# Kernel tuning notes

Measured on AMD Instinct MI355X. Metric: run time of the kernel, lower is better.

## Reference

```python
import jax, jax.numpy as jnp
import numpy as np

BUCKET_SIZE = 64
N_HASHES = 8
TOKEN_SELF_ATTN_VALUE = -50000.0


def setup_inputs() -> dict:
    key = jax.random.key(0)
    k1, k2, k3, k4 = jax.random.split(key, 4)
    b, t, h, e = 2, 4096, 8, 64
    n_buckets = t // BUCKET_SIZE  # 64
    return {
        "qk": jax.random.normal(k1, (b, t, h, e), dtype=jnp.float32),
        "k": jax.random.normal(k2, (b, t, h, e), dtype=jnp.float32),
        "v": jax.random.normal(k3, (b, t, h, e), dtype=jnp.float32),
        # shared rotations: (dim, n_hashes, n_buckets // 2)
        "rotations": jax.random.normal(k4, (e, N_HASHES, n_buckets // 2), dtype=jnp.float32),
    }


def _look_one_back(x):
    # cat([x[:, -1:], x[:, :-1]], 1) == roll by 1 along chunk axis
    return jnp.concatenate([x, jnp.roll(x, 1, axis=1)], axis=2)


def reference(qk, k, v, rotations):
    b, t, h, e = qk.shape
    # 'b t h e -> (b h) t e'
    qk_m = qk.transpose(0, 2, 1, 3).reshape(b * h, t, e)
    v_m = v.transpose(0, 2, 1, 3).reshape(b * h, t, v.shape[-1])
    B, seqlen, dim = qk_m.shape
    dv = v_m.shape[-1]
    n_buckets = seqlen // BUCKET_SIZE

    # --- LSH hashing ---
    rot = jnp.einsum('btf,fhi->bhti', qk_m, rotations)  # (B, n_hashes, T, nb/2)
    rot = jnp.concatenate([rot, -rot], axis=-1)
    buckets = jnp.argmax(rot, axis=-1)                  # (B, n_hashes, T)
    offsets = (jnp.arange(N_HASHES) * n_buckets)[None, :, None]
    buckets = (buckets + offsets).reshape(B, -1)        # (B, n_hashes*T)

    # --- sort by bucket (keys are unique, so order is deterministic) ---
    ticker = jnp.arange(N_HASHES * seqlen)[None, :]
    buckets_and_t = seqlen * buckets + (ticker % seqlen)
    sticker = jnp.argsort(buckets_and_t, axis=-1)
    undo_sort = jnp.argsort(sticker, axis=-1)
    st = sticker % seqlen

    sqk = jnp.take_along_axis(qk_m, st[:, :, None], axis=1)
    sv = jnp.take_along_axis(v_m, st[:, :, None], axis=1)

    chunk = N_HASHES * n_buckets
    bq_t = st.reshape(B, chunk, -1)                     # (B, C, bs)
    bq = sqk.reshape(B, chunk, -1, dim)                 # (B, C, bs, e)
    bv = sv.reshape(B, chunk, -1, dv)

    # normalized keys (F.normalize with eps=1e-12)
    norm = jnp.maximum(jnp.linalg.norm(bq, axis=-1, keepdims=True), 1e-12)
    bk = bq / norm

    bk = _look_one_back(bk)
    bv2 = _look_one_back(bv)
    bkv_t = _look_one_back(bq_t)

    dots = jnp.einsum('bcie,bcje->bcij', bq, bk)        # (B, C, bs, 2*bs)
    self_mask = bq_t[:, :, :, None] == bkv_t[:, :, None, :]
    dots = jnp.where(self_mask, TOKEN_SELF_ATTN_VALUE, dots)

    lse = jax.nn.logsumexp(dots, axis=-1, keepdims=True)
    p = jnp.exp(dots - lse)
    bo = jnp.einsum('bcij,bcjd->bcid', p, bv2)

    so = bo.reshape(B, -1, dv)
    slogits = lse.reshape(B, -1)
    o = jnp.take_along_axis(so, undo_sort[:, :, None], axis=1)
    logits = jnp.take_along_axis(slogits, undo_sort, axis=1)

    o = o.reshape(B, N_HASHES, seqlen, dv)
    logits = logits.reshape(B, N_HASHES, seqlen, 1)

    # combine across hash rounds by softmax over round logsumexps
    probs = jnp.exp(logits - jax.nn.logsumexp(logits, axis=1, keepdims=True))
    out = jnp.sum(o * probs, axis=1)                    # (b*h, T, dv)
    return out
```

## Files before the change

### kernel.cpp

```cpp
#include <hip/hip_runtime.h>
#include <stdint.h>

#define BHN 16
#define TLEN 4096
#define EDIM 64
#define NHASH 8
#define NBUCK 64
#define GBUCK 512
#define NCHUNK 512
#define NITEMS 32768

#define WS_BUCKETS 0u
#define WS_SORTED  557056u
#define WS_LSE     2654208u
#define WS_O       4751360u
#define WS_QK16    71860224u
#define WS_V16     80248832u
#define WS_NQ      88637440u
#define WS_RTH     114065408u
#define WS_RTM     114098176u
#define WS_RTL     114130944u

typedef __attribute__((ext_vector_type(4))) float f32x4;
typedef __attribute__((ext_vector_type(8))) _Float16 f16x8;
typedef __attribute__((ext_vector_type(4))) _Float16 f16x4;
typedef __attribute__((ext_vector_type(4))) unsigned u32x4;

#define LOG2E 1.44269504088896f
#define LN2   0.69314718055995f
#define S11   4.8828125e-4f
#define S22   2.384185791015625e-7f

static __device__ __forceinline__ void split3(float x, _Float16& h0, _Float16& m0, _Float16& l0) {
  h0 = (_Float16)x;
  float r1 = x - (float)h0;
  m0 = (_Float16)(r1 * 2048.0f);
  float r2 = r1 - (float)m0 * (1.0f / 2048.0f);
  l0 = (_Float16)(r2 * 4194304.0f);
}

__global__ __launch_bounds__(128) void k_prep(const float* __restrict__ qk,
                                              const float* __restrict__ vin,
                                              const float* __restrict__ rot,
                                              _Float16* __restrict__ qk16n,
                                              _Float16* __restrict__ v16,
                                              float* __restrict__ nq,
                                              _Float16* __restrict__ rth,
                                              _Float16* __restrict__ rtm,
                                              _Float16* __restrict__ rtl) {
  int blk = blockIdx.x;
  int tid = threadIdx.x;

  if (blk == 8192) {
#pragma unroll
    for (int rep = 0; rep < 2; ++rep) {
      int n = tid + rep * 128;
      for (int f = 0; f < 64; ++f) {
        float x = rot[f * 256 + n];
        _Float16 h0, m0, l0;
        split3(x, h0, m0, l0);
        rth[n * 64 + f] = h0;
        rtm[n * 64 + f] = m0;
        rtl[n * 64 + f] = l0;
      }
    }
    return;
  }

  int b = blk >> 12, t = blk & 4095;
  int h = tid >> 4, e4 = tid & 15;

  size_t in_base = ((size_t)((b * 4096 + t) * 8 + h)) * 64 + e4 * 4;
  float4 qv = *(const float4*)(qk + in_base);
  float ss = qv.x * qv.x + qv.y * qv.y + qv.z * qv.z + qv.w * qv.w;
  ss += __shfl_xor(ss, 1);
  ss += __shfl_xor(ss, 2);
  ss += __shfl_xor(ss, 4);
  ss += __shfl_xor(ss, 8);
  float nrm = fmaxf(sqrtf(ss), 1e-12f);
  float inv = 1.f / nrm;

  size_t out_base = ((size_t)((b * 8 + h) * 4096 + t)) * 64 + e4 * 4;
  f16x4 qh;
  qh[0] = (_Float16)(qv.x * inv); qh[1] = (_Float16)(qv.y * inv);
  qh[2] = (_Float16)(qv.z * inv); qh[3] = (_Float16)(qv.w * inv);
  *(f16x4*)(qk16n + out_base) = qh;
  if (e4 == 0) nq[(size_t)(b * 8 + h) * 4096 + t] = nrm * LOG2E;

  float4 vv = *(const float4*)(vin + in_base);
  f16x4 vh;
  vh[0] = (_Float16)vv.x; vh[1] = (_Float16)vv.y;
  vh[2] = (_Float16)vv.z; vh[3] = (_Float16)vv.w;
  *(f16x4*)(v16 + out_base) = vh;
}

__global__ __launch_bounds__(256) void k_hash2(const float* __restrict__ qk,
                                               const _Float16* __restrict__ rth,
                                               const _Float16* __restrict__ rtm,
                                               const _Float16* __restrict__ rtl,
                                               uint8_t* __restrict__ buckets) {
  __shared__ __attribute__((aligned(16))) _Float16 ah[64 * 64];
  __shared__ __attribute__((aligned(16))) _Float16 am[64 * 64];
  __shared__ __attribute__((aligned(16))) _Float16 al[64 * 64];

  int tid = threadIdx.x;
  int bh = blockIdx.x >> 6;
  int tt = blockIdx.x & 63;
  int b = bh >> 3, head = bh & 7;

  {
    int r = tid & 63, fq = tid >> 6;
    const float4* src = (const float4*)(qk +
        ((size_t)((b * 4096 + tt * 64 + r) * 8 + head)) * 64 + fq * 16);
    float x[16];
#pragma unroll
    for (int i = 0; i < 4; ++i) {
      float4 v = src[i];
      x[4 * i + 0] = v.x; x[4 * i + 1] = v.y;
      x[4 * i + 2] = v.z; x[4 * i + 3] = v.w;
    }
    int s0 = fq * 2, rx = r & 7;
#pragma unroll
    for (int g8 = 0; g8 < 2; ++g8) {
      f16x8 hv, mv, lv;
#pragma unroll
      for (int e = 0; e < 8; ++e) {
        _Float16 h0, m0, l0;
        split3(x[g8 * 8 + e], h0, m0, l0);
        hv[e] = h0; mv[e] = m0; lv[e] = l0;
      }
      int off = r * 64 + (((s0 + g8) ^ rx) << 3);
      *(f16x8*)&ah[off] = hv;
      *(f16x8*)&am[off] = mv;
      *(f16x8*)&al[off] = lv;
    }
  }
  __syncthreads();

  int w = tid >> 6, l = tid & 63;
  int col = l & 15, kg = l >> 4;

  float bv[4][4];
  int   bi[4][4];

#pragma unroll
  for (int nt = 0; nt < 4; ++nt) {
    int nrow = w * 64 + nt * 16 + col;
    const _Float16* bh_p = rth + nrow * 64 + kg * 8;
    const _Float16* bm_p = rtm + nrow * 64 + kg * 8;
    const _Float16* bl_p = rtl + nrow * 64 + kg * 8;
    f16x8 Bh0 = *(const f16x8*)(bh_p),      Bh1 = *(const f16x8*)(bh_p + 32);
    f16x8 Bm0 = *(const f16x8*)(bm_p),      Bm1 = *(const f16x8*)(bm_p + 32);
    f16x8 Bl0 = *(const f16x8*)(bl_p),      Bl1 = *(const f16x8*)(bl_p + 32);

    f32x4 C0[4], C1[4], C2[4];
#pragma unroll
    for (int mt = 0; mt < 4; ++mt) {
      C0[mt] = (f32x4){0.f, 0.f, 0.f, 0.f};
      C1[mt] = (f32x4){0.f, 0.f, 0.f, 0.f};
      C2[mt] = (f32x4){0.f, 0.f, 0.f, 0.f};
    }

    __builtin_amdgcn_s_setprio(1);
#pragma unroll
    for (int mt = 0; mt < 4; ++mt) {
      int ar = mt * 16 + col, arx = ar & 7;
#pragma unroll
      for (int kh = 0; kh < 2; ++kh) {
        int slot = kh * 4 + kg;
        f16x8 Ah = *(f16x8*)&ah[ar * 64 + ((slot ^ arx) << 3)];
        f16x8 Am = *(f16x8*)&am[ar * 64 + ((slot ^ arx) << 3)];
        f16x8 Al = *(f16x8*)&al[ar * 64 + ((slot ^ arx) << 3)];
        f16x8 Bh = kh ? Bh1 : Bh0;
        f16x8 Bm = kh ? Bm1 : Bm0;
        f16x8 Bl = kh ? Bl1 : Bl0;
        C2[mt] = __builtin_amdgcn_mfma_f32_16x16x32_f16(Ah, Bl, C2[mt], 0, 0, 0);
        C2[mt] = __builtin_amdgcn_mfma_f32_16x16x32_f16(Al, Bh, C2[mt], 0, 0, 0);
        C2[mt] = __builtin_amdgcn_mfma_f32_16x16x32_f16(Am, Bm, C2[mt], 0, 0, 0);
        C1[mt] = __builtin_amdgcn_mfma_f32_16x16x32_f16(Ah, Bm, C1[mt], 0, 0, 0);
        C1[mt] = __builtin_amdgcn_mfma_f32_16x16x32_f16(Am, Bh, C1[mt], 0, 0, 0);
        C0[mt] = __builtin_amdgcn_mfma_f32_16x16x32_f16(Ah, Bh, C0[mt], 0, 0, 0);
      }
    }
    __builtin_amdgcn_s_setprio(0);

    int ib = (nt & 1) * 16 + col;
#pragma unroll
    for (int mt = 0; mt < 4; ++mt) {
#pragma unroll
      for (int r = 0; r < 4; ++r) {
        float V = C0[mt][r] + C1[mt][r] * S11 + C2[mt][r] * S22;
        float av = fabsf(V);
        int fi = (V >= 0.f) ? ib : ib + 32;
        if ((nt & 1) == 0) {
          bv[mt][r] = av; bi[mt][r] = fi;
        } else {
          if (av > bv[mt][r] || (av == bv[mt][r] && fi < bi[mt][r])) {
            bv[mt][r] = av; bi[mt][r] = fi;
          }
        }
      }
    }

    if (nt & 1) {
      int h = w * 2 + (nt >> 1);
#pragma unroll
      for (int mt = 0; mt < 4; ++mt) {
#pragma unroll
        for (int r = 0; r < 4; ++r) {
          float v = bv[mt][r]; int i_ = bi[mt][r];
#pragma unroll
          for (int d = 1; d < 16; d <<= 1) {
            float ov = __shfl_xor(v, d);
            int   oi = __shfl_xor(i_, d);
            if (ov > v || (ov == v && oi < i_)) { v = ov; i_ = oi; }
          }
          if (col == 0) {
            int t = tt * 64 + mt * 16 + kg * 4 + r;
            buckets[(bh * 8 + h) * 4096 + t] = (uint8_t)i_;
          }
        }
      }
    }
  }
}

__global__ __launch_bounds__(64) void k_sort(const uint8_t* __restrict__ buckets,
                                             int* __restrict__ sorted) {
  __shared__ uint8_t bkt[4096];
  __shared__ uint8_t lrk[4096];
  __shared__ int hist[64 * 65];
  __shared__ int sbase[64];
  int tid = threadIdx.x;
  int bh = blockIdx.x >> 3, h = blockIdx.x & 7;

  const int* src = (const int*)(buckets + (size_t)(bh * 8 + h) * 4096);
  for (int k = tid; k < 1024; k += 64) ((int*)bkt)[k] = src[k];
  for (int k = tid; k < 64 * 65; k += 64) hist[k] = 0;
  __syncthreads();

  {
    int c = tid;
    for (int k = 0; k < 64; ++k) {
      int t = c * 64 + k;
      int bin = bkt[t];
      int r = hist[c * 65 + bin];
      hist[c * 65 + bin] = r + 1;
      lrk[t] = (uint8_t)r;
    }
  }
  __syncthreads();

  int run = 0;
  {
    int bb = tid;
    for (int c2 = 0; c2 < 64; ++c2) {
      int val = hist[c2 * 65 + bb];
      hist[c2 * 65 + bb] = run;
      run += val;
    }
  }
  {
    int ex = run;
#pragma unroll
    for (int d = 1; d < 64; d <<= 1) {
      int o = __shfl_up(ex, d);
      if (tid >= d) ex += o;
    }
    ex -= run;
    sbase[tid] = h * 4096 + ex;
  }
  __syncthreads();

  {
    int c = tid;
    int* dst = sorted + (size_t)bh * 32768;
    for (int k = 0; k < 64; ++k) {
      int t = c * 64 + k;
      int bin = bkt[t];
      int pos = sbase[bin] + hist[c * 65 + bin] + (int)lrk[t];
      dst[pos] = h * 4096 + t;
    }
  }
}

__global__ __launch_bounds__(256, 4) void k_attn(const _Float16* __restrict__ qk16n,
                                                 const _Float16* __restrict__ v16,
                                                 const float* __restrict__ nq,
                                                 const int* __restrict__ sorted,
                                                 _Float16* __restrict__ o_buf,
                                                 float* __restrict__ lse_buf) {
  __shared__ __attribute__((aligned(16))) _Float16 kf[128 * 64];
  __shared__ __attribute__((aligned(16))) _Float16 vt[64 * 128];
  __shared__ __attribute__((aligned(16))) float pinv_s[64];
  __shared__ __attribute__((aligned(16))) int tv[128];
  __shared__ __attribute__((aligned(16))) int items[64];

  int tid = threadIdx.x;
  int bh = blockIdx.x & 15;
  int c  = blockIdx.x >> 4;

  if (tid < 128) {
    int r = tid;
    int pos = (r < 64) ? (c * 64 + r) : (((c + 511) & 511) * 64 + (r - 64));
    int item = sorted[(size_t)bh * 32768 + pos];
    tv[r] = item & 4095;
    if (r < 64) items[r] = item;
  }
  __syncthreads();

  int w = tid >> 6;
  int l = tid & 63;
  int col = l & 15;
  int kg = l >> 4;
  int rq = w * 16 + col;
  int rqx7 = rq & 7, rqx15 = rq & 15;
  int tq = tv[rq];
  float nqv = nq[(size_t)bh * 4096 + tq];

  {
    int r = tid >> 1, half = tid & 1;
    int t = tv[r];
    const f16x8* src = (const f16x8*)(qk16n + ((size_t)(bh * 4096 + t)) * 64 + half * 32);
    f16x8 d0 = src[0], d1 = src[1], d2 = src[2], d3 = src[3];
    int rx = r & 7, s0 = half * 4;
    *(f16x8*)&kf[r * 64 + (((s0 + 0) ^ rx) << 3)] = d0;
    *(f16x8*)&kf[r * 64 + (((s0 + 1) ^ rx) << 3)] = d1;
    *(f16x8*)&kf[r * 64 + (((s0 + 2) ^ rx) << 3)] = d2;
    *(f16x8*)&kf[r * 64 + (((s0 + 3) ^ rx) << 3)] = d3;
  }

  {
    int jp = tid & 63, db = tid >> 6, f0 = db * 16;
    int t0 = tv[2 * jp], t1 = tv[2 * jp + 1];
    const u32x4* s0p = (const u32x4*)(v16 + ((size_t)(bh * 4096 + t0)) * 64 + f0);
    const u32x4* s1p = (const u32x4*)(v16 + ((size_t)(bh * 4096 + t1)) * 64 + f0);
    u32x4 lo0 = s0p[0], hi0 = s0p[1];
    u32x4 lo1 = s1p[0], hi1 = s1p[1];
    int jbase = ((jp >> 2));
    int joff = (jp & 3) << 1;
#pragma unroll
    for (int i = 0; i < 16; ++i) {
      int d = f0 + i;
      unsigned a = (i < 8) ? lo0[(i >> 1) & 3] : hi0[(i >> 1) & 3];
      unsigned bsrc = (i < 8) ? lo1[(i >> 1) & 3] : hi1[(i >> 1) & 3];
      unsigned sel = (i & 1) ? 0x07060302u : 0x05040100u;
      unsigned pack = __builtin_amdgcn_perm(bsrc, a, sel);
      *(unsigned*)&vt[d * 128 + ((jbase ^ (d & 15)) << 3) + joff] = pack;
    }
  }
  __syncthreads();

  f16x8 qf[2];
#pragma unroll
  for (int ks = 0; ks < 2; ++ks)
    qf[ks] = *(f16x8*)&kf[rq * 64 + (((ks * 4 + kg) ^ rqx7) << 3)];

  f32x4 S[8];
#pragma unroll
  for (int mt = 0; mt < 8; ++mt) S[mt] = (f32x4){0.f, 0.f, 0.f, 0.f};

  __builtin_amdgcn_s_setprio(1);
#pragma unroll
  for (int mt = 0; mt < 8; ++mt) {
    int rj = mt * 16 + col;
    int rjx = rj & 7;
#pragma unroll
    for (int ks = 0; ks < 2; ++ks) {
      f16x8 a = *(f16x8*)&kf[rj * 64 + (((ks * 4 + kg) ^ rjx) << 3)];
      S[mt] = __builtin_amdgcn_mfma_f32_16x16x32_f16(a, qf[ks], S[mt], 0, 0, 0);
    }
  }
  __builtin_amdgcn_s_setprio(0);

  float vals[32];
  float mx = -1e30f;
#pragma unroll
  for (int mt = 0; mt < 8; ++mt) {
    int j0 = mt * 16 + kg * 4;
    int4 tk4 = *(int4*)&tv[j0];
    int tki[4] = {tk4.x, tk4.y, tk4.z, tk4.w};
#pragma unroll
    for (int r = 0; r < 4; ++r) {
      float d = S[mt][r] * nqv;
      if (tki[r] == tq) d = -50000.0f * LOG2E;
      vals[mt * 4 + r] = d;
      mx = fmaxf(mx, d);
    }
  }
  mx = fmaxf(mx, __shfl_xor(mx, 16));
  mx = fmaxf(mx, __shfl_xor(mx, 32));
  float ssum = 0.f;
#pragma unroll
  for (int i = 0; i < 32; ++i) {
    float e = __builtin_amdgcn_exp2f(vals[i] - mx);
    vals[i] = e;
    ssum += e;
  }
  ssum += __shfl_xor(ssum, 16);
  ssum += __shfl_xor(ssum, 32);
  if (kg == 0) {
    int item = items[rq];
    lse_buf[((size_t)bh * 4096 + (item & 4095)) * 8 + (item >> 12)] =
        (mx + __builtin_amdgcn_logf(ssum)) * LN2;
    pinv_s[rq] = 1.f / ssum;
  }

  __syncthreads();

  _Float16* Pb = kf;
#pragma unroll
  for (int mt = 0; mt < 8; ++mt) {
    int j0 = mt * 16 + kg * 4;
    int slot = j0 >> 3;
    int off = rq * 128 + ((slot ^ rqx15) << 3) + ((kg & 1) << 2);
    f16x4 pk;
#pragma unroll
    for (int r = 0; r < 4; ++r) pk[r] = (_Float16)vals[mt * 4 + r];
    *(f16x4*)&Pb[off] = pk;
  }
  asm volatile("s_waitcnt lgkmcnt(0)" ::: "memory");

  f32x4 O[4];
#pragma unroll
  for (int nt = 0; nt < 4; ++nt) O[nt] = (f32x4){0.f, 0.f, 0.f, 0.f};
  __builtin_amdgcn_s_setprio(1);
#pragma unroll
  for (int ks = 0; ks < 4; ++ks) {
    int slot = (ks << 2) + kg;
    f16x8 pa = *(f16x8*)&Pb[rq * 128 + ((slot ^ rqx15) << 3)];
#pragma unroll
    for (int nt = 0; nt < 4; ++nt) {
      int dD = nt * 16 + col;
      f16x8 vb = *(f16x8*)&vt[dD * 128 + ((slot ^ (dD & 15)) << 3)];
      O[nt] = __builtin_amdgcn_mfma_f32_16x16x32_f16(pa, vb, O[nt], 0, 0, 0);
    }
  }
  __builtin_amdgcn_s_setprio(0);

  {
    int i0 = w * 16 + kg * 4;
    int4 it4 = *(int4*)&items[i0];
    float4 pv4 = *(float4*)&pinv_s[i0];
    int iti[4] = {it4.x, it4.y, it4.z, it4.w};
    float pvi[4] = {pv4.x, pv4.y, pv4.z, pv4.w};
#pragma unroll
    for (int r = 0; r < 4; ++r) {
      int item = iti[r];
      _Float16* orow = o_buf +
          (((size_t)bh * 4096 + (item & 4095)) * 8 + (item >> 12)) * 64;
#pragma unroll
      for (int nt = 0; nt < 4; ++nt) orow[nt * 16 + col] = (_Float16)(O[nt][r] * pvi[r]);
    }
  }
}

__global__ __launch_bounds__(256) void k_combine(const _Float16* __restrict__ o_buf,
                                                 const float* __restrict__ lse_buf,
                                                 float* __restrict__ out) {
  int gid = blockIdx.x * 256 + threadIdx.x;
  int d4 = gid & 15;
  int t  = (gid >> 4) & 4095;
  int bh = gid >> 16;

  const float* lrow = lse_buf + ((size_t)bh * 4096 + t) * 8;
  float lx[8];
#pragma unroll
  for (int h = 0; h < 8; ++h) lx[h] = lrow[h];
  float m = lx[0];
#pragma unroll
  for (int h = 1; h < 8; ++h) m = fmaxf(m, lx[h]);
  float wv[8]; float s = 0.f;
#pragma unroll
  for (int h = 0; h < 8; ++h) { wv[h] = __expf(lx[h] - m); s += wv[h]; }
  float inv = 1.f / s;

  const _Float16* obase = o_buf + ((size_t)bh * 4096 + t) * 8 * 64 + d4 * 4;
  float ax = 0.f, ay = 0.f, az = 0.f, aw = 0.f;
#pragma unroll
  for (int h = 0; h < 8; ++h) {
    f16x4 ov = *(const f16x4*)(obase + h * 64);
    ax = fmaf(wv[h], (float)ov[0], ax);
    ay = fmaf(wv[h], (float)ov[1], ay);
    az = fmaf(wv[h], (float)ov[2], az);
    aw = fmaf(wv[h], (float)ov[3], aw);
  }
  *(float4*)(out + ((size_t)(bh * 4096 + t)) * 64 + d4 * 4) =
      make_float4(ax * inv, ay * inv, az * inv, aw * inv);
}

extern "C" void kernel_launch(void* const* d_in, const int* in_sizes, int n_in,
                              void* d_out, int out_size, void* d_ws, size_t ws_size,
                              hipStream_t stream) {
  const float* qk  = (const float*)d_in[0];
  const float* vin = (const float*)d_in[2];
  const float* rot = (const float*)d_in[3];

  uint8_t* ws = (uint8_t*)d_ws;
  uint8_t*  buckets = ws + WS_BUCKETS;
  int*      sorted  = (int*)(ws + WS_SORTED);
  float*    lse_buf = (float*)(ws + WS_LSE);
  _Float16* o_buf   = (_Float16*)(ws + WS_O);
  _Float16* qk16n   = (_Float16*)(ws + WS_QK16);
  _Float16* v16     = (_Float16*)(ws + WS_V16);
  float*    nqbuf   = (float*)(ws + WS_NQ);
  _Float16* rth     = (_Float16*)(ws + WS_RTH);
  _Float16* rtm     = (_Float16*)(ws + WS_RTM);
  _Float16* rtl     = (_Float16*)(ws + WS_RTL);
  float*    out     = (float*)d_out;

  k_prep<<<8193, 128, 0, stream>>>(qk, vin, rot, qk16n, v16, nqbuf, rth, rtm, rtl);
  k_hash2<<<BHN * 64, 256, 0, stream>>>(qk, rth, rtm, rtl, buckets);
  k_sort<<<BHN * NHASH, 64, 0, stream>>>(buckets, sorted);
  k_attn<<<BHN * NCHUNK, 256, 0, stream>>>(qk16n, v16, nqbuf, sorted, o_buf, lse_buf);
  k_combine<<<4096, 256, 0, stream>>>(o_buf, lse_buf, out);
}
```

Measured before the change: 138.7 us.

## Fuse qk normalization and v fp16 conversion into the hash kernel

The per-token prep work (qk L2 normalization to fp16, norm output, v conversion to fp16) moves into k_hash2, which already loads the qk tile, so qk is read from global memory once instead of twice. Row norms are reduced through a small shared array. The rotation split becomes its own small, fully parallel kernel instead of one serial block inside k_prep. Each hash block now does more memory work before its MFMA loop, which may lengthen that kernel.

```diff
diff --git a/kernel.cpp b/kernel.cpp
--- a/kernel.cpp
+++ b/kernel.cpp
@@ -39,86 +39,71 @@
   l0 = (_Float16)(r2 * 4194304.0f);
 }
 
-__global__ __launch_bounds__(128) void k_prep(const float* __restrict__ qk,
-                                              const float* __restrict__ vin,
-                                              const float* __restrict__ rot,
-                                              _Float16* __restrict__ qk16n,
-                                              _Float16* __restrict__ v16,
-                                              float* __restrict__ nq,
-                                              _Float16* __restrict__ rth,
-                                              _Float16* __restrict__ rtm,
-                                              _Float16* __restrict__ rtl) {
-  int blk = blockIdx.x;
-  int tid = threadIdx.x;
-
-  if (blk == 8192) {
-#pragma unroll
-    for (int rep = 0; rep < 2; ++rep) {
-      int n = tid + rep * 128;
-      for (int f = 0; f < 64; ++f) {
-        float x = rot[f * 256 + n];
-        _Float16 h0, m0, l0;
-        split3(x, h0, m0, l0);
-        rth[n * 64 + f] = h0;
-        rtm[n * 64 + f] = m0;
-        rtl[n * 64 + f] = l0;
-      }
-    }
-    return;
-  }
-
-  int b = blk >> 12, t = blk & 4095;
-  int h = tid >> 4, e4 = tid & 15;
-
-  size_t in_base = ((size_t)((b * 4096 + t) * 8 + h)) * 64 + e4 * 4;
-  float4 qv = *(const float4*)(qk + in_base);
-  float ss = qv.x * qv.x + qv.y * qv.y + qv.z * qv.z + qv.w * qv.w;
-  ss += __shfl_xor(ss, 1);
-  ss += __shfl_xor(ss, 2);
-  ss += __shfl_xor(ss, 4);
-  ss += __shfl_xor(ss, 8);
-  float nrm = fmaxf(sqrtf(ss), 1e-12f);
-  float inv = 1.f / nrm;
-
-  size_t out_base = ((size_t)((b * 8 + h) * 4096 + t)) * 64 + e4 * 4;
-  f16x4 qh;
-  qh[0] = (_Float16)(qv.x * inv); qh[1] = (_Float16)(qv.y * inv);
-  qh[2] = (_Float16)(qv.z * inv); qh[3] = (_Float16)(qv.w * inv);
-  *(f16x4*)(qk16n + out_base) = qh;
-  if (e4 == 0) nq[(size_t)(b * 8 + h) * 4096 + t] = nrm * LOG2E;
-
-  float4 vv = *(const float4*)(vin + in_base);
-  f16x4 vh;
-  vh[0] = (_Float16)vv.x; vh[1] = (_Float16)vv.y;
-  vh[2] = (_Float16)vv.z; vh[3] = (_Float16)vv.w;
-  *(f16x4*)(v16 + out_base) = vh;
+__global__ __launch_bounds__(256) void k_rotsplit(const float* __restrict__ rot,
+                                                  _Float16* __restrict__ rth,
+                                                  _Float16* __restrict__ rtm,
+                                                  _Float16* __restrict__ rtl) {
+  int f = blockIdx.x;
+  int n = threadIdx.x;
+  float x = rot[f * 256 + n];
+  _Float16 h0, m0, l0;
+  split3(x, h0, m0, l0);
+  rth[n * 64 + f] = h0;
+  rtm[n * 64 + f] = m0;
+  rtl[n * 64 + f] = l0;
 }
 
 __global__ __launch_bounds__(256) void k_hash2(const float* __restrict__ qk,
+                                               const float* __restrict__ vin,
                                                const _Float16* __restrict__ rth,
                                                const _Float16* __restrict__ rtm,
                                                const _Float16* __restrict__ rtl,
-                                               uint8_t* __restrict__ buckets) {
+                                               uint8_t* __restrict__ buckets,
+                                               _Float16* __restrict__ qk16n,
+                                               _Float16* __restrict__ v16,
+                                               float* __restrict__ nq) {
   __shared__ __attribute__((aligned(16))) _Float16 ah[64 * 64];
   __shared__ __attribute__((aligned(16))) _Float16 am[64 * 64];
   __shared__ __attribute__((aligned(16))) _Float16 al[64 * 64];
+  __shared__ float rsum[256];
 
   int tid = threadIdx.x;
   int bh = blockIdx.x >> 6;
   int tt = blockIdx.x & 63;
   int b = bh >> 3, head = bh & 7;
 
-  {
-    int r = tid & 63, fq = tid >> 6;
-    const float4* src = (const float4*)(qk +
-        ((size_t)((b * 4096 + tt * 64 + r) * 8 + head)) * 64 + fq * 16);
-    float x[16];
+  int r = tid & 63, fq = tid >> 6;
+  size_t inbase = ((size_t)((b * 4096 + tt * 64 + r) * 8 + head)) * 64 + fq * 16;
+  size_t obase  = ((size_t)(bh * 4096 + tt * 64 + r)) * 64 + fq * 16;
+
+  float x[16];
+  {
+    const float4* srcq = (const float4*)(qk + inbase);
+    float ss = 0.f;
 #pragma unroll
     for (int i = 0; i < 4; ++i) {
-      float4 v = src[i];
+      float4 v = srcq[i];
       x[4 * i + 0] = v.x; x[4 * i + 1] = v.y;
       x[4 * i + 2] = v.z; x[4 * i + 3] = v.w;
-    }
+      ss = fmaf(v.x, v.x, ss); ss = fmaf(v.y, v.y, ss);
+      ss = fmaf(v.z, v.z, ss); ss = fmaf(v.w, v.w, ss);
+    }
+    rsum[tid] = ss;
+  }
+  {
+    const float4* srcv = (const float4*)(vin + inbase);
+#pragma unroll
+    for (int g8 = 0; g8 < 2; ++g8) {
+      float4 a = srcv[2 * g8], bb2 = srcv[2 * g8 + 1];
+      f16x8 vh;
+      vh[0] = (_Float16)a.x;  vh[1] = (_Float16)a.y;
+      vh[2] = (_Float16)a.z;  vh[3] = (_Float16)a.w;
+      vh[4] = (_Float16)bb2.x; vh[5] = (_Float16)bb2.y;
+      vh[6] = (_Float16)bb2.z; vh[7] = (_Float16)bb2.w;
+      *(f16x8*)(v16 + obase + g8 * 8) = vh;
+    }
+  }
+  {
     int s0 = fq * 2, rx = r & 7;
 #pragma unroll
     for (int g8 = 0; g8 < 2; ++g8) {
@@ -136,6 +121,20 @@
     }
   }
   __syncthreads();
+
+  {
+    float tot = rsum[r] + rsum[64 + r] + rsum[128 + r] + rsum[192 + r];
+    float nrm = fmaxf(sqrtf(tot), 1e-12f);
+    float inv = 1.f / nrm;
+#pragma unroll
+    for (int g8 = 0; g8 < 2; ++g8) {
+      f16x8 qh;
+#pragma unroll
+      for (int e = 0; e < 8; ++e) qh[e] = (_Float16)(x[g8 * 8 + e] * inv);
+      *(f16x8*)(qk16n + obase + g8 * 8) = qh;
+    }
+    if (fq == 0) nq[(size_t)bh * 4096 + tt * 64 + r] = nrm * LOG2E;
+  }
 
   int w = tid >> 6, l = tid & 63;
   int col = l & 15, kg = l >> 4;
@@ -188,15 +187,15 @@
 #pragma unroll
     for (int mt = 0; mt < 4; ++mt) {
 #pragma unroll
-      for (int r = 0; r < 4; ++r) {
-        float V = C0[mt][r] + C1[mt][r] * S11 + C2[mt][r] * S22;
+      for (int r2 = 0; r2 < 4; ++r2) {
+        float V = C0[mt][r2] + C1[mt][r2] * S11 + C2[mt][r2] * S22;
         float av = fabsf(V);
         int fi = (V >= 0.f) ? ib : ib + 32;
         if ((nt & 1) == 0) {
-          bv[mt][r] = av; bi[mt][r] = fi;
+          bv[mt][r2] = av; bi[mt][r2] = fi;
         } else {
-          if (av > bv[mt][r] || (av == bv[mt][r] && fi < bi[mt][r])) {
-            bv[mt][r] = av; bi[mt][r] = fi;
+          if (av > bv[mt][r2] || (av == bv[mt][r2] && fi < bi[mt][r2])) {
+            bv[mt][r2] = av; bi[mt][r2] = fi;
           }
         }
       }
@@ -207,8 +206,8 @@
 #pragma unroll
       for (int mt = 0; mt < 4; ++mt) {
 #pragma unroll
-        for (int r = 0; r < 4; ++r) {
-          float v = bv[mt][r]; int i_ = bi[mt][r];
+        for (int r2 = 0; r2 < 4; ++r2) {
+          float v = bv[mt][r2]; int i_ = bi[mt][r2];
 #pragma unroll
           for (int d = 1; d < 16; d <<= 1) {
             float ov = __shfl_xor(v, d);
@@ -216,7 +215,7 @@
             if (ov > v || (ov == v && oi < i_)) { v = ov; i_ = oi; }
           }
           if (col == 0) {
-            int t = tt * 64 + mt * 16 + kg * 4 + r;
+            int t = tt * 64 + mt * 16 + kg * 4 + r2;
             buckets[(bh * 8 + h) * 4096 + t] = (uint8_t)i_;
           }
         }
@@ -509,8 +508,9 @@
   _Float16* rtl     = (_Float16*)(ws + WS_RTL);
   float*    out     = (float*)d_out;
 
-  k_prep<<<8193, 128, 0, stream>>>(qk, vin, rot, qk16n, v16, nqbuf, rth, rtm, rtl);
-  k_hash2<<<BHN * 64, 256, 0, stream>>>(qk, rth, rtm, rtl, buckets);
+  k_rotsplit<<<64, 256, 0, stream>>>(rot, rth, rtm, rtl);
+  k_hash2<<<BHN * 64, 256, 0, stream>>>(qk, vin, rth, rtm, rtl, buckets,
+                                        qk16n, v16, nqbuf);
   k_sort<<<BHN * NHASH, 64, 0, stream>>>(buckets, sorted);
   k_attn<<<BHN * NCHUNK, 256, 0, stream>>>(qk16n, v16, nqbuf, sorted, o_buf, lse_buf);
   k_combine<<<4096, 256, 0, stream>>>(o_buf, lse_buf, out);
```

New measurement: 127.4 us. 8.2% less time.
